# Kernel tuning notes

Measured on AMD Instinct MI355X. Metric: run time of the kernel, lower is better.

Reference implementation:

```python
import jax, jax.numpy as jnp
import numpy as np

T = 262144          # total packed neighbor tokens
D_IN, D_H, D_OUT = 128, 256, 128
N_SETS = 8192


def setup_inputs() -> dict:
    key = jax.random.key(0)
    k1, k2, k3, k4, k5, k6 = jax.random.split(key, 6)
    x = jax.random.normal(k1, (T, D_IN), dtype=jnp.float32)
    segment_ids = jnp.sort(jax.random.randint(k2, (T,), 0, N_SETS))
    # phi params (torch Linear: y = x @ W.T + b); store as [in, out] for einsum
    s1 = 1.0 / np.sqrt(D_IN)
    s2 = 1.0 / np.sqrt(D_H)
    W1 = jax.random.uniform(k3, (D_IN, D_H), jnp.float32, -s1, s1)
    b1 = jax.random.uniform(k4, (D_H,), jnp.float32, -s1, s1)
    W2 = jax.random.uniform(k5, (D_H, D_OUT), jnp.float32, -s2, s2)
    b2 = jax.random.uniform(k6, (D_OUT,), jnp.float32, -s2, s2)
    return {"x": x, "segment_ids": segment_ids, "num_segments": N_SETS,
            "W1": W1, "b1": b1, "W2": W2, "b2": b2}


def reference(x, segment_ids, num_segments, W1, b1, W2, b2):
    # phi: Linear -> ReLU -> Linear -> ReLU, applied to every packed token
    h = jax.nn.relu(x @ W1 + b1)            # [T, D_H]
    h = jax.nn.relu(h @ W2 + b2)            # [T, D_OUT]
    # per-set mean pool (segment mean over ragged sets)
    sums = jax.ops.segment_sum(h, segment_ids, num_segments=num_segments)  # [N, D_OUT]
    counts = jax.ops.segment_sum(jnp.ones((h.shape[0],), h.dtype), segment_ids,
                                 num_segments=num_segments)                 # [N]
    out = sums / jnp.maximum(counts, 1.0)[:, None]
    return out
```

## Files before the change

kernel.cpp:

```cpp
#include <hip/hip_runtime.h>

#define D_IN 128
#define D_H 256
#define D_OUT 128
#define N_SETS 8192

typedef short short8 __attribute__((ext_vector_type(8)));
typedef short short4v __attribute__((ext_vector_type(4)));
typedef float floatx4 __attribute__((ext_vector_type(4)));

__device__ inline unsigned short f32_bf16(float f) {
    unsigned int u = __float_as_uint(f);
    u += 0x7FFFu + ((u >> 16) & 1u);
    return (unsigned short)(u >> 16);
}

__global__ void setup_kernel(const float* __restrict__ W1, const float* __restrict__ W2,
                             unsigned short* __restrict__ W1s, unsigned short* __restrict__ W2s,
                             float4* __restrict__ out4, float4* __restrict__ cnt4) {
    if (blockIdx.x < 32) {
        int t = blockIdx.x * 256 + threadIdx.x;
        int l = t & 63;
        int f = (t >> 6) & 63;
        int q = l >> 4, r = l & 15;
        if (t < 4096) {
            int nt = f >> 2, c = f & 3;
            int k0 = c * 32 + q * 8, n = nt * 16 + r;
            unsigned short v[8];
#pragma unroll
            for (int j = 0; j < 8; j++) v[j] = f32_bf16(W1[(k0 + j) * D_H + n]);
#pragma unroll
            for (int j = 0; j < 8; j++) W1s[f * 512 + l * 8 + j] = v[j];
        } else {
            int nt = f >> 3, c = f & 7;
            int k0 = c * 32 + q * 8, n = nt * 16 + r;
            unsigned short v[8];
#pragma unroll
            for (int j = 0; j < 8; j++) v[j] = f32_bf16(W2[(k0 + j) * D_OUT + n]);
#pragma unroll
            for (int j = 0; j < 8; j++) W2s[f * 512 + l * 8 + j] = v[j];
        }
    } else {
        int i = (blockIdx.x - 32) * 256 + threadIdx.x;
        float4 z = make_float4(0.f, 0.f, 0.f, 0.f);
        if (i < 262144) out4[i] = z;
        else if (i < 264192) cnt4[i - 262144] = z;
    }
}

__global__ __launch_bounds__(256, 3) void ds_main(
    const float* __restrict__ x, const int* __restrict__ seg,
    const unsigned short* __restrict__ W1s, const float* __restrict__ b1,
    const unsigned short* __restrict__ W2s, const float* __restrict__ b2,
    float* __restrict__ out, float* __restrict__ counts)
{
    __shared__ unsigned short slabs[4][1280];
    __shared__ int ssegs[4][32];

    const int tid = threadIdx.x;
    const int wave = tid >> 6, lane = tid & 63;
    const int r = lane & 15, q = lane >> 4;
    const int tok0 = blockIdx.x * 128 + wave * 32;

    unsigned short* slab = slabs[wave];
    int* sseg = ssegs[wave];
    if (lane < 32) sseg[lane] = seg[tok0 + lane];

    short8 xfb[2][4];
#pragma unroll
    for (int mt = 0; mt < 2; mt++) {
        const float* xp = x + (size_t)(tok0 + mt * 16 + r) * D_IN + q * 8;
#pragma unroll
        for (int c = 0; c < 4; c++) {
            float4 v0 = *(const float4*)(xp + c * 32);
            float4 v1 = *(const float4*)(xp + c * 32 + 4);
            short8 w;
            w[0] = (short)f32_bf16(v0.x); w[1] = (short)f32_bf16(v0.y);
            w[2] = (short)f32_bf16(v0.z); w[3] = (short)f32_bf16(v0.w);
            w[4] = (short)f32_bf16(v1.x); w[5] = (short)f32_bf16(v1.y);
            w[6] = (short)f32_bf16(v1.z); w[7] = (short)f32_bf16(v1.w);
            xfb[mt][c] = w;
        }
    }

    floatx4 acc2[8][2];
#pragma unroll
    for (int i = 0; i < 8; i++) {
        acc2[i][0] = (floatx4){0.f, 0.f, 0.f, 0.f};
        acc2[i][1] = (floatx4){0.f, 0.f, 0.f, 0.f};
    }

#pragma unroll
    for (int kc = 0; kc < 8; kc++) {
#pragma unroll
        for (int t = 0; t < 2; t++) {
            const int nt = kc * 2 + t;
            short8 w1f[4];
#pragma unroll
            for (int c = 0; c < 4; c++)
                w1f[c] = *(const short8*)(W1s + (nt * 4 + c) * 512 + lane * 8);
            floatx4 b1v = *(const floatx4*)(b1 + nt * 16 + q * 4);
            floatx4 acc1[2];
            acc1[0] = (floatx4){0.f, 0.f, 0.f, 0.f};
            acc1[1] = (floatx4){0.f, 0.f, 0.f, 0.f};
#pragma unroll
            for (int c = 0; c < 4; c++) {
                acc1[0] = __builtin_amdgcn_mfma_f32_16x16x32_bf16(w1f[c], xfb[0][c], acc1[0], 0, 0, 0);
                acc1[1] = __builtin_amdgcn_mfma_f32_16x16x32_bf16(w1f[c], xfb[1][c], acc1[1], 0, 0, 0);
            }
#pragma unroll
            for (int mt = 0; mt < 2; mt++) {
                short4v pk;
#pragma unroll
                for (int i = 0; i < 4; i++)
                    pk[i] = (short)f32_bf16(fmaxf(acc1[mt][i] + b1v[i], 0.f));
                *(short4v*)(slab + (mt * 16 + r) * 40 + t * 16 + q * 4) = pk;
            }
        }
        short8 a2[2];
        a2[0] = *(const short8*)(slab + r * 40 + q * 8);
        a2[1] = *(const short8*)(slab + (16 + r) * 40 + q * 8);
#pragma unroll
        for (int nt2 = 0; nt2 < 8; nt2++) {
            short8 bw = *(const short8*)(W2s + (nt2 * 8 + kc) * 512 + lane * 8);
            acc2[nt2][0] = __builtin_amdgcn_mfma_f32_16x16x32_bf16(a2[0], bw, acc2[nt2][0], 0, 0, 0);
            acc2[nt2][1] = __builtin_amdgcn_mfma_f32_16x16x32_bf16(a2[1], bw, acc2[nt2][1], 0, 0, 0);
        }
    }

    if (lane < 32) {
        int s = sseg[lane];
        if (lane == 0 || sseg[lane - 1] != s) {
            int len = 1;
            for (int u = lane + 1; u < 32 && sseg[u] == s; ++u) ++len;
            atomicAdd(&counts[s], (float)len);
        }
    }

    int sid[8];
#pragma unroll
    for (int e = 0; e < 8; e++) sid[e] = sseg[q * 8 + e];

    float* h2 = (float*)slab;
#pragma unroll
    for (int nt2 = 0; nt2 < 8; nt2++) {
        const float bias = b2[nt2 * 16 + r];
#pragma unroll
        for (int mt = 0; mt < 2; mt++) {
            floatx4 v;
#pragma unroll
            for (int i = 0; i < 4; i++) v[i] = fmaxf(acc2[nt2][mt][i] + bias, 0.f);
            *(floatx4*)(h2 + r * 36 + mt * 16 + q * 4) = v;
        }
        floatx4 v0 = *(const floatx4*)(h2 + r * 36 + q * 8);
        floatx4 v1 = *(const floatx4*)(h2 + r * 36 + q * 8 + 4);
        const int col = nt2 * 16 + r;
        float sum = v0[0];
#pragma unroll
        for (int e = 1; e < 8; e++) {
            float v = (e < 4) ? v0[e] : v1[e - 4];
            if (sid[e] != sid[e - 1]) {
                atomicAdd(&out[(size_t)sid[e - 1] * D_OUT + col], sum);
                sum = 0.f;
            }
            sum += v;
        }
        atomicAdd(&out[(size_t)sid[7] * D_OUT + col], sum);
    }
}

__global__ void div_kernel(float4* __restrict__ out4, const float* __restrict__ counts) {
    int i = blockIdx.x * 256 + threadIdx.x;
    float inv = 1.f / fmaxf(counts[i >> 5], 1.f);
    float4 v = out4[i];
    v.x *= inv; v.y *= inv; v.z *= inv; v.w *= inv;
    out4[i] = v;
}

extern "C" void kernel_launch(void* const* d_in, const int* in_sizes, int n_in,
                              void* d_out, int out_size, void* d_ws, size_t ws_size,
                              hipStream_t stream) {
    const float* x  = (const float*)d_in[0];
    const int* seg  = (const int*)d_in[1];
    const float* W1 = (const float*)d_in[3];
    const float* b1 = (const float*)d_in[4];
    const float* W2 = (const float*)d_in[5];
    const float* b2 = (const float*)d_in[6];
    float* out = (float*)d_out;

    float* counts       = (float*)d_ws;
    unsigned short* W1s = (unsigned short*)((char*)d_ws + 32768);
    unsigned short* W2s = (unsigned short*)((char*)d_ws + 32768 + 65536);

    hipLaunchKernelGGL(setup_kernel, dim3(1064), dim3(256), 0, stream,
                       W1, W2, W1s, W2s, (float4*)out, (float4*)counts);
    hipLaunchKernelGGL(ds_main, dim3(2048), dim3(256), 0, stream,
                       x, seg, W1s, b1, W2s, b2, out, counts);
    hipLaunchKernelGGL(div_kernel, dim3(1024), dim3(256), 0, stream,
                       (float4*)out, counts);
}
```

Before: 303.2 us.

## Stage weight fragments through double-buffered LDS via async global_load_lds

Instead of each wave reading the swizzled W1/W2 bf16 fragments directly from global memory, the block cooperatively copies each k-chunk's 16 fragments into a double-buffered LDS area with global_load_lds, prefetching the next chunk while computing the current one. The intent is to cut the redundant per-wave global/L2 traffic for weights by a factor of four and to hide load latency. In exchange it adds 32 KB of LDS per block, which may reduce occupancy below the launch-bounds target, and it adds a block-wide barrier every iteration. There is also no explicit vmcnt wait before the barrier, so correctness depends on the compiler inserting one for the async LDS loads.

```diff
diff --git a/kernel.cpp b/kernel.cpp
--- a/kernel.cpp
+++ b/kernel.cpp
@@ -8,6 +8,9 @@
 typedef short short8 __attribute__((ext_vector_type(8)));
 typedef short short4v __attribute__((ext_vector_type(4)));
 typedef float floatx4 __attribute__((ext_vector_type(4)));
+
+typedef const __attribute__((address_space(1))) unsigned int gu32;
+typedef __attribute__((address_space(3))) unsigned int lu32;
 
 __device__ inline unsigned short f32_bf16(float f) {
     unsigned int u = __float_as_uint(f);
@@ -54,13 +57,24 @@
     const unsigned short* __restrict__ W2s, const float* __restrict__ b2,
     float* __restrict__ out, float* __restrict__ counts)
 {
-    __shared__ unsigned short slabs[4][1280];
+    __shared__ __align__(16) unsigned short wbuf[2][16 * 512];
+    __shared__ __align__(16) unsigned short slabs[4][1280];
     __shared__ int ssegs[4][32];
 
     const int tid = threadIdx.x;
     const int wave = tid >> 6, lane = tid & 63;
     const int r = lane & 15, q = lane >> 4;
     const int tok0 = blockIdx.x * 128 + wave * 32;
+
+#pragma unroll
+    for (int i = 0; i < 4; i++) {
+        const int f = wave * 4 + i;
+        const unsigned short* src = (f < 8) ? (W1s + (0 * 8 + f) * 512)
+                                            : (W2s + ((f - 8) * 8 + 0) * 512);
+        __builtin_amdgcn_global_load_lds((gu32*)(src + lane * 8),
+                                         (lu32*)(&wbuf[0][f * 512] + lane * 8),
+                                         16, 0, 0);
+    }
 
     unsigned short* slab = slabs[wave];
     int* sseg = ssegs[wave];
@@ -90,15 +104,33 @@
         acc2[i][1] = (floatx4){0.f, 0.f, 0.f, 0.f};
     }
 
+    __syncthreads();
+
 #pragma unroll
     for (int kc = 0; kc < 8; kc++) {
+        const unsigned short* wb = wbuf[kc & 1];
+
+        if (kc < 7) {
+            const int kn = kc + 1;
+            unsigned short* wn = wbuf[kn & 1];
+#pragma unroll
+            for (int i = 0; i < 4; i++) {
+                const int f = wave * 4 + i;
+                const unsigned short* src = (f < 8) ? (W1s + (kn * 8 + f) * 512)
+                                                    : (W2s + ((f - 8) * 8 + kn) * 512);
+                __builtin_amdgcn_global_load_lds((gu32*)(src + lane * 8),
+                                                 (lu32*)(wn + f * 512 + lane * 8),
+                                                 16, 0, 0);
+            }
+        }
+
 #pragma unroll
         for (int t = 0; t < 2; t++) {
             const int nt = kc * 2 + t;
             short8 w1f[4];
 #pragma unroll
             for (int c = 0; c < 4; c++)
-                w1f[c] = *(const short8*)(W1s + (nt * 4 + c) * 512 + lane * 8);
+                w1f[c] = *(const short8*)(wb + (t * 4 + c) * 512 + lane * 8);
             floatx4 b1v = *(const floatx4*)(b1 + nt * 16 + q * 4);
             floatx4 acc1[2];
             acc1[0] = (floatx4){0.f, 0.f, 0.f, 0.f};
@@ -122,10 +154,12 @@
         a2[1] = *(const short8*)(slab + (16 + r) * 40 + q * 8);
 #pragma unroll
         for (int nt2 = 0; nt2 < 8; nt2++) {
-            short8 bw = *(const short8*)(W2s + (nt2 * 8 + kc) * 512 + lane * 8);
+            short8 bw = *(const short8*)(wb + (8 + nt2) * 512 + lane * 8);
             acc2[nt2][0] = __builtin_amdgcn_mfma_f32_16x16x32_bf16(a2[0], bw, acc2[nt2][0], 0, 0, 0);
             acc2[nt2][1] = __builtin_amdgcn_mfma_f32_16x16x32_bf16(a2[1], bw, acc2[nt2][1], 0, 0, 0);
         }
+
+        if (kc < 7) __syncthreads();
     }
 
     if (lane < 32) {
```

Measured after the change: 268.8 us. 11.3% less time.
